# Kernel tuning notes

Measured on AMD Instinct MI355X. Metric: run time of the kernel, lower is better.

Reference implementation:

```python
import jax, jax.numpy as jnp
import numpy as np

NCLS, NDF, B = 256, 512, 1024
ALP = 0.1


def setup_inputs() -> dict:
    key = jax.random.key(0)
    k1, k2, k3 = jax.random.split(key, 3)
    df = jax.random.normal(k1, (B, NDF), dtype=jnp.float32)
    gt = jax.random.randint(k2, (B,), 0, NCLS)
    fc = jax.random.normal(k3, (NCLS, NDF), dtype=jnp.float32)
    return {"df": df, "gt": gt, "fc": fc}


def _update_stats(df, gt):
    """Sequential per-sample running mean/var update (moving_avg=False branch).
    Faithful to the torch no_grad loop: per-class counter `it`, c1=it/(it+1),
    c2=1/(it+1); mean[t]=f when it==0 else mean[t]*c1+f*c2;
    var[t]=var[t]*c1 + (f-mean[t])**2 * c1*c2. Buffers start at zero.
    """
    mean0 = jnp.zeros((NCLS, NDF), jnp.float32)
    var0 = jnp.zeros((NCLS, NDF), jnp.float32)
    it0 = jnp.zeros((NCLS,), jnp.int32)

    def step(carry, xt):
        mean, var, it = carry
        f, t = xt
        n = it[t]
        nf = n.astype(jnp.float32)
        c1 = nf / (nf + 1.0)
        c2 = 1.0 / (nf + 1.0)
        m_t = jnp.where(n == 0, f, mean[t] * c1 + f * c2)
        a = (f - m_t) ** 2
        v_t = var[t] * c1 + a * c1 * c2
        return (mean.at[t].set(m_t), var.at[t].set(v_t), it.at[t].add(1)), None

    (mean, var, it), _ = jax.lax.scan(step, (mean0, var0, it0), (df, gt))
    return mean, var


def reference(df, gt, fc):
    # stats updated from detached features (torch uses no_grad)
    _, var = _update_stats(jax.lax.stop_gradient(df), gt)
    Var = var[gt]          # (B, ndf)
    Fc = fc[gt]            # (B, ndf): column of fc for each sample's class
    W = fc[None, :, :] - Fc[:, None, :]  # (B, ncls, ndf)
    # score[b,c] = W[b,c,:].df[b,:] + alp/2 * (W**2)[b,c,:].Var[b,:]
    score = jnp.einsum('bcd,bd->bc', W, df) \
        + 0.5 * ALP * jnp.einsum('bcd,bd->bc', W * W, Var)
    return score[:, :, None]  # (B, ncls, 1), matching torch matmul output
```

## Files before the change

### kernel.cpp

```cpp
#include <hip/hip_runtime.h>

#define NCLS 256
#define NDF  512
#define BSZ  1024
#define ALP  0.1f
#define LSTR 68


__device__ __forceinline__ void gemm_inner(const float (*As)[LSTR], const float (*Bs)[LSTR],
                                           int tx, int ty, float4* acc) {
#pragma unroll
    for (int kk = 0; kk < 32; ++kk) {
        const float4 a = *(const float4*)&As[kk][ty * 4];
        const float4 b = *(const float4*)&Bs[kk][tx * 4];
        acc[0].x += a.x * b.x; acc[0].y += a.x * b.y; acc[0].z += a.x * b.z; acc[0].w += a.x * b.w;
        acc[1].x += a.y * b.x; acc[1].y += a.y * b.y; acc[1].z += a.y * b.z; acc[1].w += a.y * b.w;
        acc[2].x += a.z * b.x; acc[2].y += a.z * b.y; acc[2].z += a.z * b.z; acc[2].w += a.z * b.w;
        acc[3].x += a.w * b.x; acc[3].y += a.w * b.y; acc[3].z += a.w * b.z; acc[3].w += a.w * b.w;
    }
}

__global__ __launch_bounds__(256) void fused_main(const float* __restrict__ df,
                                                  const int* __restrict__ gt,
                                                  const float* __restrict__ fc,
                                                  float* __restrict__ s1p,
                                                  float* __restrict__ Rp) {
    __shared__ float As[32][LSTR];
    __shared__ float Bs[32][LSTR];
    __shared__ int gts[BSZ];
    __shared__ unsigned long long bmap[64 * 16];

    const int tid = threadIdx.x;
    const int bid = blockIdx.x;
    const int tx = tid & 15, ty = tid >> 4;

    float4 acc[4];
    acc[0] = make_float4(0.f, 0.f, 0.f, 0.f);
    acc[1] = acc[0]; acc[2] = acc[0]; acc[3] = acc[0];

    if (bid < 256) {
        const int z = bid & 3;
        const int tile = bid >> 2;
        const int bm = tile & 15, bn = tile >> 4;
        const int arow = tid >> 2;
        const int kq = (tid & 3) << 3;
        const float* Ag = df + (bm * 64 + arow) * NDF + z * 128 + kq;
        const float* Bg = fc + (bn * 64 + arow) * NDF + z * 128 + kq;

        float4 a0 = *(const float4*)Ag, a1 = *(const float4*)(Ag + 4);
        float4 b0 = *(const float4*)Bg, b1 = *(const float4*)(Bg + 4);
#pragma unroll 1
        for (int ks = 0; ks < 4; ++ks) {
            __syncthreads();
            As[kq + 0][arow] = a0.x; As[kq + 1][arow] = a0.y; As[kq + 2][arow] = a0.z; As[kq + 3][arow] = a0.w;
            As[kq + 4][arow] = a1.x; As[kq + 5][arow] = a1.y; As[kq + 6][arow] = a1.z; As[kq + 7][arow] = a1.w;
            Bs[kq + 0][arow] = b0.x; Bs[kq + 1][arow] = b0.y; Bs[kq + 2][arow] = b0.z; Bs[kq + 3][arow] = b0.w;
            Bs[kq + 4][arow] = b1.x; Bs[kq + 5][arow] = b1.y; Bs[kq + 6][arow] = b1.z; Bs[kq + 7][arow] = b1.w;
            __syncthreads();
            if (ks < 3) {
                const int off = (ks + 1) * 32;
                a0 = *(const float4*)(Ag + off); a1 = *(const float4*)(Ag + off + 4);
                b0 = *(const float4*)(Bg + off); b1 = *(const float4*)(Bg + off + 4);
            }
            gemm_inner(As, Bs, tx, ty, acc);
        }
        float* Cp = s1p + z * (BSZ * NCLS) + (bm * 64 + ty * 4) * NCLS + bn * 64 + tx * 4;
#pragma unroll
        for (int i = 0; i < 4; ++i) *(float4*)(Cp + i * NCLS) = acc[i];
    } else {
        const int r = bid - 256;
        const int z = r & 7;
        const int tile = r >> 3;
        const int bm = tile & 3, bn = tile >> 2;
        const int D0 = z * 64;
        const int clocal = tid >> 2;
        const int dg = tid & 3;
        const int myclass = bm * 64 + clocal;
        const int dim0 = D0 + dg * 16;

        for (int i = tid; i < BSZ; i += 256) gts[i] = gt[i];
        for (int i = tid; i < 1024; i += 256) bmap[i] = 0ull;
        __syncthreads();
        for (int i = tid; i < BSZ; i += 256) {
            const int c = gts[i] - bm * 64;
            if ((unsigned)c < 64u) atomicOr(&bmap[c * 16 + (i >> 6)], 1ull << (i & 63));
        }
        const float* fct = fc + myclass * NDF + dim0;
        float fcq[16];
        {
            const float4 q0 = ((const float4*)fct)[0], q1 = ((const float4*)fct)[1];
            const float4 q2 = ((const float4*)fct)[2], q3 = ((const float4*)fct)[3];
            fcq[0]=q0.x; fcq[1]=q0.y; fcq[2]=q0.z; fcq[3]=q0.w;
            fcq[4]=q1.x; fcq[5]=q1.y; fcq[6]=q1.z; fcq[7]=q1.w;
            fcq[8]=q2.x; fcq[9]=q2.y; fcq[10]=q2.z; fcq[11]=q2.w;
            fcq[12]=q3.x; fcq[13]=q3.y; fcq[14]=q3.z; fcq[15]=q3.w;
        }
        __syncthreads();

        float m[16], v[16];
#pragma unroll
        for (int j = 0; j < 16; ++j) { m[j] = 0.f; v[j] = 0.f; }
        float nf = 0.f;
        {
            int w = 0;
            unsigned long long bits = bmap[clocal * 16];
            auto next = [&]() -> int {
                while (bits == 0ull) {
                    if (w >= 15) return -1;
                    bits = bmap[clocal * 16 + (++w)];
                }
                const int b = __ffsll((unsigned long long)bits) - 1;
                bits &= bits - 1ull;
                return (w << 6) + b;
            };
            int cur = next();
            float f[16];
            if (cur >= 0) {
                const float* p = df + cur * NDF + dim0;
                const float4 q0 = ((const float4*)p)[0], q1 = ((const float4*)p)[1];
                const float4 q2 = ((const float4*)p)[2], q3 = ((const float4*)p)[3];
                f[0]=q0.x; f[1]=q0.y; f[2]=q0.z; f[3]=q0.w;
                f[4]=q1.x; f[5]=q1.y; f[6]=q1.z; f[7]=q1.w;
                f[8]=q2.x; f[9]=q2.y; f[10]=q2.z; f[11]=q2.w;
                f[12]=q3.x; f[13]=q3.y; f[14]=q3.z; f[15]=q3.w;
            }
            while (cur >= 0) {
                const int nxt = next();
                float g[16];
                if (nxt >= 0) {
                    const float* p = df + nxt * NDF + dim0;
                    const float4 q0 = ((const float4*)p)[0], q1 = ((const float4*)p)[1];
                    const float4 q2 = ((const float4*)p)[2], q3 = ((const float4*)p)[3];
                    g[0]=q0.x; g[1]=q0.y; g[2]=q0.z; g[3]=q0.w;
                    g[4]=q1.x; g[5]=q1.y; g[6]=q1.z; g[7]=q1.w;
                    g[8]=q2.x; g[9]=q2.y; g[10]=q2.z; g[11]=q2.w;
                    g[12]=q3.x; g[13]=q3.y; g[14]=q3.z; g[15]=q3.w;
                }
                const float c2 = 1.0f / (nf + 1.0f);
                const float c1 = nf * c2;
                const float c12 = c1 * c2;
#pragma unroll
                for (int j = 0; j < 16; ++j) {
                    m[j] = m[j] * c1 + f[j] * c2;
                    const float a = f[j] - m[j];
                    v[j] = v[j] * c1 + a * a * c12;
                }
                nf += 1.0f;
#pragma unroll
                for (int j = 0; j < 16; ++j) f[j] = g[j];
                cur = nxt;
            }
        }

        const int crow = tid >> 2, kq = (tid & 3) << 3;
        const float* Bg = fc + (bn * 64 + crow) * NDF + D0;
        float4 b0 = *(const float4*)(Bg + kq), b1 = *(const float4*)(Bg + kq + 4);
#pragma unroll 1
        for (int ks = 0; ks < 4; ++ks) {
            const bool quad = (ks >= 2);
            float4 w0 = b0, w1 = b1;
            if (quad) {
                w0.x *= w0.x; w0.y *= w0.y; w0.z *= w0.z; w0.w *= w0.w;
                w1.x *= w1.x; w1.y *= w1.y; w1.z *= w1.z; w1.w *= w1.w;
            }
            __syncthreads();
            if ((dg >> 1) == (ks & 1)) {
                const int kb = (dg & 1) * 16;
#pragma unroll
                for (int j = 0; j < 16; ++j) {
                    As[kb + j][clocal] = quad ? v[j] : (-2.f * fcq[j] * v[j]);
                }
            }
            Bs[kq + 0][crow] = w0.x; Bs[kq + 1][crow] = w0.y; Bs[kq + 2][crow] = w0.z; Bs[kq + 3][crow] = w0.w;
            Bs[kq + 4][crow] = w1.x; Bs[kq + 5][crow] = w1.y; Bs[kq + 6][crow] = w1.z; Bs[kq + 7][crow] = w1.w;
            __syncthreads();
            if (ks < 3) {
                const int off = ((ks + 1) & 1) * 32;
                b0 = *(const float4*)(Bg + off + kq);
                b1 = *(const float4*)(Bg + off + kq + 4);
            }
            gemm_inner(As, Bs, tx, ty, acc);
        }
        float* Cp = Rp + z * (NCLS * NCLS) + (bm * 64 + ty * 4) * NCLS + bn * 64 + tx * 4;
#pragma unroll
        for (int i = 0; i < 4; ++i) *(float4*)(Cp + i * NCLS) = acc[i];
    }
}

__global__ __launch_bounds__(256) void epilogue_kernel(const float* __restrict__ s1p,
                                                       const float* __restrict__ Rp,
                                                       const int* __restrict__ gt,
                                                       float* __restrict__ out) {
    __shared__ float sv1[NCLS];
    __shared__ float svR[NCLS];
    const int b = blockIdx.x;
    const int c = threadIdx.x;
    const int t = gt[b];
    float v1 = 0.f;
#pragma unroll
    for (int zz = 0; zz < 4; ++zz) v1 += s1p[zz * (BSZ * NCLS) + b * NCLS + c];
    float vR = 0.f;
#pragma unroll
    for (int zz = 0; zz < 8; ++zz) vR += Rp[zz * (NCLS * NCLS) + t * NCLS + c];
    sv1[c] = v1;
    svR[c] = vR;
    __syncthreads();
    out[b * NCLS + c] = (v1 - sv1[t]) + 0.5f * ALP * (vR - svR[t]);
}

extern "C" void kernel_launch(void* const* d_in, const int* in_sizes, int n_in,
                              void* d_out, int out_size, void* d_ws, size_t ws_size,
                              hipStream_t stream) {
    const float* df = (const float*)d_in[0];
    const int* gt = (const int*)d_in[1];
    const float* fc = (const float*)d_in[2];
    float* out = (float*)d_out;

    float* ws = (float*)d_ws;
    float* s1p = ws;
    float* Rp = s1p + 4 * BSZ * NCLS;

    fused_main<<<384, 256, 0, stream>>>(df, gt, fc, s1p, Rp);
    epilogue_kernel<<<BSZ, 256, 0, stream>>>(s1p, Rp, gt, out);
}
```

Baseline: 29.64 us.

## Fuse stats, GEMMs and epilogue into one bf16 MFMA kernel

Replaces the two-kernel design (fp32 SIMT GEMMs with split-K partials plus an epilogue reduction) with a single kernel. Each block computes a 32x32 output tile using bf16 MFMA 16x16x32 instructions and swizzled LDS tiles. Every block recomputes the per-sample running variance for its 32 samples, and the diagonal bias terms are folded in directly, so the partial-sum workspace and the second launch go away. The cost is bf16 rounding error, and the variance work is repeated across the 8 column blocks.

```diff
diff --git a/kernel.cpp b/kernel.cpp
--- a/kernel.cpp
+++ b/kernel.cpp
@@ -4,110 +4,124 @@
 #define NDF  512
 #define BSZ  1024
 #define ALP  0.1f
-#define LSTR 68
-
-
-__device__ __forceinline__ void gemm_inner(const float (*As)[LSTR], const float (*Bs)[LSTR],
-                                           int tx, int ty, float4* acc) {
-#pragma unroll
-    for (int kk = 0; kk < 32; ++kk) {
-        const float4 a = *(const float4*)&As[kk][ty * 4];
-        const float4 b = *(const float4*)&Bs[kk][tx * 4];
-        acc[0].x += a.x * b.x; acc[0].y += a.x * b.y; acc[0].z += a.x * b.z; acc[0].w += a.x * b.w;
-        acc[1].x += a.y * b.x; acc[1].y += a.y * b.y; acc[1].z += a.y * b.z; acc[1].w += a.y * b.w;
-        acc[2].x += a.z * b.x; acc[2].y += a.z * b.y; acc[2].z += a.z * b.z; acc[2].w += a.z * b.w;
-        acc[3].x += a.w * b.x; acc[3].y += a.w * b.y; acc[3].z += a.w * b.z; acc[3].w += a.w * b.w;
-    }
-}
-
-__global__ __launch_bounds__(256) void fused_main(const float* __restrict__ df,
-                                                  const int* __restrict__ gt,
-                                                  const float* __restrict__ fc,
-                                                  float* __restrict__ s1p,
-                                                  float* __restrict__ Rp) {
-    __shared__ float As[32][LSTR];
-    __shared__ float Bs[32][LSTR];
-    __shared__ int gts[BSZ];
-    __shared__ unsigned long long bmap[64 * 16];
+
+
+typedef __attribute__((ext_vector_type(8))) short bf16x8;
+typedef __attribute__((ext_vector_type(4))) float f32x4;
+
+__device__ __forceinline__ unsigned rne_pk(float lo, float hi) {
+    union { float f; unsigned u; } a, b;
+    a.f = lo; b.f = hi;
+    unsigned ua = (a.u + 0x7FFFu + ((a.u >> 16) & 1u)) >> 16;
+    unsigned ub = (b.u + 0x7FFFu + ((b.u >> 16) & 1u)) & 0xFFFF0000u;
+    return ua | ub;
+}
+__device__ __forceinline__ uint4 pk16(float4 p, float4 q) {
+    uint4 r;
+    r.x = rne_pk(p.x, p.y); r.y = rne_pk(p.z, p.w);
+    r.z = rne_pk(q.x, q.y); r.w = rne_pk(q.z, q.w);
+    return r;
+}
+__device__ __forceinline__ uint4 pk8a(const float* x) {
+    uint4 r;
+    r.x = rne_pk(x[0], x[1]); r.y = rne_pk(x[2], x[3]);
+    r.z = rne_pk(x[4], x[5]); r.w = rne_pk(x[6], x[7]);
+    return r;
+}
+__device__ __forceinline__ float bf16r(float x) {
+    union { float f; unsigned u; } c; c.f = x;
+    c.u = (c.u + 0x7FFFu + ((c.u >> 16) & 1u)) & 0xFFFF0000u;
+    return c.f;
+}
+__device__ __forceinline__ void unpk4(float* o, float4 q) {
+    o[0] = q.x; o[1] = q.y; o[2] = q.z; o[3] = q.w;
+}
+
+__global__ __launch_bounds__(256) void fused_one(const float* __restrict__ df,
+                                                 const int* __restrict__ gt,
+                                                 const float* __restrict__ fc,
+                                                 float* __restrict__ out) {
+    __shared__ union {
+        struct {
+            alignas(16) char dfT[32 * 256];
+            alignas(16) char fcT[32 * 256];
+            alignas(16) char alT[32 * 256];
+            alignas(16) char aqT[32 * 256];
+            alignas(16) char bqT[32 * 256];
+        } t;
+        struct { unsigned long long bmap[256 * 16]; int gts[BSZ]; } p;
+    } sm;
+    __shared__ unsigned long long slotmap[32 * 16];
+    __shared__ float biasL[32], rttL[32];
 
     const int tid = threadIdx.x;
-    const int bid = blockIdx.x;
-    const int tx = tid & 15, ty = tid >> 4;
-
-    float4 acc[4];
-    acc[0] = make_float4(0.f, 0.f, 0.f, 0.f);
-    acc[1] = acc[0]; acc[2] = acc[0]; acc[3] = acc[0];
-
-    if (bid < 256) {
-        const int z = bid & 3;
-        const int tile = bid >> 2;
-        const int bm = tile & 15, bn = tile >> 4;
-        const int arow = tid >> 2;
-        const int kq = (tid & 3) << 3;
-        const float* Ag = df + (bm * 64 + arow) * NDF + z * 128 + kq;
-        const float* Bg = fc + (bn * 64 + arow) * NDF + z * 128 + kq;
-
-        float4 a0 = *(const float4*)Ag, a1 = *(const float4*)(Ag + 4);
-        float4 b0 = *(const float4*)Bg, b1 = *(const float4*)(Bg + 4);
+    const int bm = blockIdx.x >> 3, bn = blockIdx.x & 7;
+    const int slot = tid >> 3, ln8 = tid & 7;
+
+    for (int i = tid; i < 256 * 16; i += 256) sm.p.bmap[i] = 0ull;
+    for (int i = tid; i < BSZ; i += 256) sm.p.gts[i] = gt[i];
+    __syncthreads();
+    for (int i = tid; i < BSZ; i += 256)
+        atomicOr(&sm.p.bmap[sm.p.gts[i] * 16 + (i >> 6)], 1ull << (i & 63));
+    __syncthreads();
+    const int myt = sm.p.gts[bm * 32 + slot];
+    for (int u = tid; u < 512; u += 256)
+        slotmap[u] = sm.p.bmap[sm.p.gts[bm * 32 + (u >> 4)] * 16 + (u & 15)];
+    __syncthreads();
+
+    const int sampleg = bm * 32 + slot;
+    const int dbyte = ln8 * 32;
+    const int swz = (slot & 7) << 4;
+    char* dfR = sm.t.dfT + slot * 256;
+    char* fcR = sm.t.fcT + slot * 256;
+    char* alR = sm.t.alT + slot * 256;
+    char* aqR = sm.t.aqT + slot * 256;
+    char* bqR = sm.t.bqT + slot * 256;
+
+    const int lane = tid & 63, wv = tid >> 6;
+    const int wm = (wv >> 1) * 16, wn = (wv & 1) * 16;
+    const int fr = lane & 15, fkb = (lane >> 4) * 16, fswz = (fr & 7) << 4;
+
+    f32x4 accS = 0.f, accR = 0.f;
+    float bias = 0.f, rtt = 0.f;
+
 #pragma unroll 1
-        for (int ks = 0; ks < 4; ++ks) {
-            __syncthreads();
-            As[kq + 0][arow] = a0.x; As[kq + 1][arow] = a0.y; As[kq + 2][arow] = a0.z; As[kq + 3][arow] = a0.w;
-            As[kq + 4][arow] = a1.x; As[kq + 5][arow] = a1.y; As[kq + 6][arow] = a1.z; As[kq + 7][arow] = a1.w;
-            Bs[kq + 0][arow] = b0.x; Bs[kq + 1][arow] = b0.y; Bs[kq + 2][arow] = b0.z; Bs[kq + 3][arow] = b0.w;
-            Bs[kq + 4][arow] = b1.x; Bs[kq + 5][arow] = b1.y; Bs[kq + 6][arow] = b1.z; Bs[kq + 7][arow] = b1.w;
-            __syncthreads();
-            if (ks < 3) {
-                const int off = (ks + 1) * 32;
-                a0 = *(const float4*)(Ag + off); a1 = *(const float4*)(Ag + off + 4);
-                b0 = *(const float4*)(Bg + off); b1 = *(const float4*)(Bg + off + 4);
-            }
-            gemm_inner(As, Bs, tx, ty, acc);
-        }
-        float* Cp = s1p + z * (BSZ * NCLS) + (bm * 64 + ty * 4) * NCLS + bn * 64 + tx * 4;
-#pragma unroll
-        for (int i = 0; i < 4; ++i) *(float4*)(Cp + i * NCLS) = acc[i];
-    } else {
-        const int r = bid - 256;
-        const int z = r & 7;
-        const int tile = r >> 3;
-        const int bm = tile & 3, bn = tile >> 2;
-        const int D0 = z * 64;
-        const int clocal = tid >> 2;
-        const int dg = tid & 3;
-        const int myclass = bm * 64 + clocal;
-        const int dim0 = D0 + dg * 16;
-
-        for (int i = tid; i < BSZ; i += 256) gts[i] = gt[i];
-        for (int i = tid; i < 1024; i += 256) bmap[i] = 0ull;
-        __syncthreads();
-        for (int i = tid; i < BSZ; i += 256) {
-            const int c = gts[i] - bm * 64;
-            if ((unsigned)c < 64u) atomicOr(&bmap[c * 16 + (i >> 6)], 1ull << (i & 63));
-        }
-        const float* fct = fc + myclass * NDF + dim0;
-        float fcq[16];
+    for (int ch = 0; ch < 4; ++ch) {
+        const int dim0 = ch * 128 + ln8 * 16;
+        const float* pd = df + sampleg * NDF + dim0;
+        const float* pc = fc + (bn * 32 + slot) * NDF + dim0;
+        const float* pt = fc + myt * NDF + dim0;
+        const float4 dv0 = ((const float4*)pd)[0], dv1 = ((const float4*)pd)[1],
+                     dv2 = ((const float4*)pd)[2], dv3 = ((const float4*)pd)[3];
+        const float4 cv0 = ((const float4*)pc)[0], cv1 = ((const float4*)pc)[1],
+                     cv2 = ((const float4*)pc)[2], cv3 = ((const float4*)pc)[3];
+        const float4 tv0 = ((const float4*)pt)[0], tv1 = ((const float4*)pt)[1],
+                     tv2 = ((const float4*)pt)[2], tv3 = ((const float4*)pt)[3];
+
+        *(uint4*)(dfR + (dbyte ^ swz)) = pk16(dv0, dv1);
+        *(uint4*)(dfR + ((dbyte + 16) ^ swz)) = pk16(dv2, dv3);
+        *(uint4*)(fcR + (dbyte ^ swz)) = pk16(cv0, cv1);
+        *(uint4*)(fcR + ((dbyte + 16) ^ swz)) = pk16(cv2, cv3);
         {
-            const float4 q0 = ((const float4*)fct)[0], q1 = ((const float4*)fct)[1];
-            const float4 q2 = ((const float4*)fct)[2], q3 = ((const float4*)fct)[3];
-            fcq[0]=q0.x; fcq[1]=q0.y; fcq[2]=q0.z; fcq[3]=q0.w;
-            fcq[4]=q1.x; fcq[5]=q1.y; fcq[6]=q1.z; fcq[7]=q1.w;
-            fcq[8]=q2.x; fcq[9]=q2.y; fcq[10]=q2.z; fcq[11]=q2.w;
-            fcq[12]=q3.x; fcq[13]=q3.y; fcq[14]=q3.z; fcq[15]=q3.w;
-        }
-        __syncthreads();
-
-        float m[16], v[16];
-#pragma unroll
-        for (int j = 0; j < 16; ++j) { m[j] = 0.f; v[j] = 0.f; }
-        float nf = 0.f;
+            float c16[16], q16[16];
+            unpk4(c16 + 0, cv0); unpk4(c16 + 4, cv1); unpk4(c16 + 8, cv2); unpk4(c16 + 12, cv3);
+#pragma unroll
+            for (int j = 0; j < 16; ++j) q16[j] = c16[j] * c16[j];
+            *(uint4*)(bqR + (dbyte ^ swz)) = pk8a(q16);
+            *(uint4*)(bqR + ((dbyte + 16) ^ swz)) = pk8a(q16 + 8);
+        }
+
+        float m16[16], v16[16];
+#pragma unroll
+        for (int j = 0; j < 16; ++j) { m16[j] = 0.f; v16[j] = 0.f; }
         {
+            float nf = 0.f;
             int w = 0;
-            unsigned long long bits = bmap[clocal * 16];
+            unsigned long long bits = slotmap[slot * 16];
             auto next = [&]() -> int {
                 while (bits == 0ull) {
                     if (w >= 15) return -1;
-                    bits = bmap[clocal * 16 + (++w)];
+                    bits = slotmap[slot * 16 + (++w)];
                 }
                 const int b = __ffsll((unsigned long long)bits) - 1;
                 bits &= bits - 1ull;
@@ -117,33 +131,25 @@
             float f[16];
             if (cur >= 0) {
                 const float* p = df + cur * NDF + dim0;
-                const float4 q0 = ((const float4*)p)[0], q1 = ((const float4*)p)[1];
-                const float4 q2 = ((const float4*)p)[2], q3 = ((const float4*)p)[3];
-                f[0]=q0.x; f[1]=q0.y; f[2]=q0.z; f[3]=q0.w;
-                f[4]=q1.x; f[5]=q1.y; f[6]=q1.z; f[7]=q1.w;
-                f[8]=q2.x; f[9]=q2.y; f[10]=q2.z; f[11]=q2.w;
-                f[12]=q3.x; f[13]=q3.y; f[14]=q3.z; f[15]=q3.w;
+                unpk4(f + 0, ((const float4*)p)[0]); unpk4(f + 4, ((const float4*)p)[1]);
+                unpk4(f + 8, ((const float4*)p)[2]); unpk4(f + 12, ((const float4*)p)[3]);
             }
             while (cur >= 0) {
                 const int nxt = next();
                 float g[16];
                 if (nxt >= 0) {
                     const float* p = df + nxt * NDF + dim0;
-                    const float4 q0 = ((const float4*)p)[0], q1 = ((const float4*)p)[1];
-                    const float4 q2 = ((const float4*)p)[2], q3 = ((const float4*)p)[3];
-                    g[0]=q0.x; g[1]=q0.y; g[2]=q0.z; g[3]=q0.w;
-                    g[4]=q1.x; g[5]=q1.y; g[6]=q1.z; g[7]=q1.w;
-                    g[8]=q2.x; g[9]=q2.y; g[10]=q2.z; g[11]=q2.w;
-                    g[12]=q3.x; g[13]=q3.y; g[14]=q3.z; g[15]=q3.w;
+                    unpk4(g + 0, ((const float4*)p)[0]); unpk4(g + 4, ((const float4*)p)[1]);
+                    unpk4(g + 8, ((const float4*)p)[2]); unpk4(g + 12, ((const float4*)p)[3]);
                 }
                 const float c2 = 1.0f / (nf + 1.0f);
                 const float c1 = nf * c2;
                 const float c12 = c1 * c2;
 #pragma unroll
                 for (int j = 0; j < 16; ++j) {
-                    m[j] = m[j] * c1 + f[j] * c2;
-                    const float a = f[j] - m[j];
-                    v[j] = v[j] * c1 + a * a * c12;
+                    m16[j] = m16[j] * c1 + f[j] * c2;
+                    const float a = f[j] - m16[j];
+                    v16[j] = v16[j] * c1 + a * a * c12;
                 }
                 nf += 1.0f;
 #pragma unroll
@@ -152,60 +158,50 @@
             }
         }
 
-        const int crow = tid >> 2, kq = (tid & 3) << 3;
-        const float* Bg = fc + (bn * 64 + crow) * NDF + D0;
-        float4 b0 = *(const float4*)(Bg + kq), b1 = *(const float4*)(Bg + kq + 4);
-#pragma unroll 1
-        for (int ks = 0; ks < 4; ++ks) {
-            const bool quad = (ks >= 2);
-            float4 w0 = b0, w1 = b1;
-            if (quad) {
-                w0.x *= w0.x; w0.y *= w0.y; w0.z *= w0.z; w0.w *= w0.w;
-                w1.x *= w1.x; w1.y *= w1.y; w1.z *= w1.z; w1.w *= w1.w;
+        {
+            float t16[16], d16[16], l16[16];
+            unpk4(t16 + 0, tv0); unpk4(t16 + 4, tv1); unpk4(t16 + 8, tv2); unpk4(t16 + 12, tv3);
+            unpk4(d16 + 0, dv0); unpk4(d16 + 4, dv1); unpk4(d16 + 8, dv2); unpk4(d16 + 12, dv3);
+#pragma unroll
+            for (int j = 0; j < 16; ++j) {
+                l16[j] = -2.f * t16[j] * v16[j];
+                bias = fmaf(bf16r(d16[j]), bf16r(t16[j]), bias);
+                rtt = fmaf(bf16r(t16[j] * t16[j]), bf16r(v16[j]), rtt);
+                rtt = fmaf(bf16r(l16[j]), bf16r(t16[j]), rtt);
             }
-            __syncthreads();
-            if ((dg >> 1) == (ks & 1)) {
-                const int kb = (dg & 1) * 16;
-#pragma unroll
-                for (int j = 0; j < 16; ++j) {
-                    As[kb + j][clocal] = quad ? v[j] : (-2.f * fcq[j] * v[j]);
-                }
-            }
-            Bs[kq + 0][crow] = w0.x; Bs[kq + 1][crow] = w0.y; Bs[kq + 2][crow] = w0.z; Bs[kq + 3][crow] = w0.w;
-            Bs[kq + 4][crow] = w1.x; Bs[kq + 5][crow] = w1.y; Bs[kq + 6][crow] = w1.z; Bs[kq + 7][crow] = w1.w;
-            __syncthreads();
-            if (ks < 3) {
-                const int off = ((ks + 1) & 1) * 32;
-                b0 = *(const float4*)(Bg + off + kq);
-                b1 = *(const float4*)(Bg + off + kq + 4);
-            }
-            gemm_inner(As, Bs, tx, ty, acc);
-        }
-        float* Cp = Rp + z * (NCLS * NCLS) + (bm * 64 + ty * 4) * NCLS + bn * 64 + tx * 4;
-#pragma unroll
-        for (int i = 0; i < 4; ++i) *(float4*)(Cp + i * NCLS) = acc[i];
+            *(uint4*)(alR + (dbyte ^ swz)) = pk8a(l16);
+            *(uint4*)(alR + ((dbyte + 16) ^ swz)) = pk8a(l16 + 8);
+            *(uint4*)(aqR + (dbyte ^ swz)) = pk8a(v16);
+            *(uint4*)(aqR + ((dbyte + 16) ^ swz)) = pk8a(v16 + 8);
+        }
+        __syncthreads();
+
+#pragma unroll
+        for (int s = 0; s < 4; ++s) {
+            const int kb = (s * 64 + fkb) ^ fswz;
+            const bf16x8 aS = *(const bf16x8*)(sm.t.dfT + (wm + fr) * 256 + kb);
+            const bf16x8 bC = *(const bf16x8*)(sm.t.fcT + (wn + fr) * 256 + kb);
+            const bf16x8 aL = *(const bf16x8*)(sm.t.alT + (wm + fr) * 256 + kb);
+            const bf16x8 aQ = *(const bf16x8*)(sm.t.aqT + (wm + fr) * 256 + kb);
+            const bf16x8 bQ = *(const bf16x8*)(sm.t.bqT + (wn + fr) * 256 + kb);
+            accS = __builtin_amdgcn_mfma_f32_16x16x32_bf16(aS, bC, accS, 0, 0, 0);
+            accR = __builtin_amdgcn_mfma_f32_16x16x32_bf16(aL, bC, accR, 0, 0, 0);
+            accR = __builtin_amdgcn_mfma_f32_16x16x32_bf16(aQ, bQ, accR, 0, 0, 0);
+        }
+        __syncthreads();
     }
-}
-
-__global__ __launch_bounds__(256) void epilogue_kernel(const float* __restrict__ s1p,
-                                                       const float* __restrict__ Rp,
-                                                       const int* __restrict__ gt,
-                                                       float* __restrict__ out) {
-    __shared__ float sv1[NCLS];
-    __shared__ float svR[NCLS];
-    const int b = blockIdx.x;
-    const int c = threadIdx.x;
-    const int t = gt[b];
-    float v1 = 0.f;
-#pragma unroll
-    for (int zz = 0; zz < 4; ++zz) v1 += s1p[zz * (BSZ * NCLS) + b * NCLS + c];
-    float vR = 0.f;
-#pragma unroll
-    for (int zz = 0; zz < 8; ++zz) vR += Rp[zz * (NCLS * NCLS) + t * NCLS + c];
-    sv1[c] = v1;
-    svR[c] = vR;
-    __syncthreads();
-    out[b * NCLS + c] = (v1 - sv1[t]) + 0.5f * ALP * (vR - svR[t]);
+
+    bias += __shfl_xor(bias, 1); bias += __shfl_xor(bias, 2); bias += __shfl_xor(bias, 4);
+    rtt += __shfl_xor(rtt, 1);   rtt += __shfl_xor(rtt, 2);   rtt += __shfl_xor(rtt, 4);
+    if (ln8 == 0) { biasL[slot] = bias; rttL[slot] = rtt; }
+    __syncthreads();
+
+#pragma unroll
+    for (int r = 0; r < 4; ++r) {
+        const int row = wm + (lane >> 4) * 4 + r;
+        out[(bm * 32 + row) * NCLS + bn * 32 + wn + fr] =
+            (accS[r] - biasL[row]) + 0.5f * ALP * (accR[r] - rttL[row]);
+    }
 }
 
 extern "C" void kernel_launch(void* const* d_in, const int* in_sizes, int n_in,
@@ -216,10 +212,5 @@
     const float* fc = (const float*)d_in[2];
     float* out = (float*)d_out;
 
-    float* ws = (float*)d_ws;
-    float* s1p = ws;
-    float* Rp = s1p + 4 * BSZ * NCLS;
-
-    fused_main<<<384, 256, 0, stream>>>(df, gt, fc, s1p, Rp);
-    epilogue_kernel<<<BSZ, 256, 0, stream>>>(s1p, Rp, gt, out);
-}
+    fused_one<<<256, 256, 0, stream>>>(df, gt, fc, out);
+}
```

Result: slower. 51.92 us (+75.2%).
